# Optimization experiments

Measured on AMD Instinct MI355X. Metric: run time of the kernel, lower is better.

## Reference

```python
import jax, jax.numpy as jnp
import numpy as np

BS, NA, NE, NAL = 512, 8, 8, 7        # batch, agents, enemies, allies
OWN_F, EN_F, AL_F = 16, 16, 16        # per-entity feature dims
H, HEADS, HYPER, OUT_N = 64, 4, 64, 6 # rnn_hidden_dim, hpn heads, hyper hidden, normal actions
D_E = (EN_F * H + H + 1) * HEADS      # hypernet-enemy out: input-layer W + fc2 W + fc2 b (per head)
D_A = AL_F * H * HEADS                # hypernet-ally out: input-layer W only (non-MMM map)


def setup_inputs() -> dict:
    key = jax.random.key(0)
    ks = jax.random.split(key, 16)
    def w(k, shape, fan):
        return jax.random.normal(k, shape, jnp.float32) / np.sqrt(fan)
    n = BS * NA
    return dict(
        own_feats=jax.random.normal(ks[0], (n, OWN_F), jnp.float32),
        enemy_feats=jax.random.normal(ks[1], (n * NE, EN_F), jnp.float32),
        ally_feats=jax.random.normal(ks[2], (n * NAL, AL_F), jnp.float32),
        hidden_state=jax.random.normal(ks[3], (n, H), jnp.float32),
        fc1_w=w(ks[4], (OWN_F, H), OWN_F), fc1_b=jnp.zeros((H,), jnp.float32),
        he_w1=w(ks[5], (EN_F, HYPER), EN_F), he_b1=jnp.zeros((HYPER,), jnp.float32),
        he_w2=w(ks[6], (HYPER, D_E), HYPER), he_b2=jnp.zeros((D_E,), jnp.float32),
        ha_w1=w(ks[7], (AL_F, HYPER), AL_F), ha_b1=jnp.zeros((HYPER,), jnp.float32),
        ha_w2=w(ks[8], (HYPER, D_A), HYPER), ha_b2=jnp.zeros((D_A,), jnp.float32),
        w_in_merge=jnp.full((HEADS, H), 1.0 / HEADS, jnp.float32),
        gru_w_ih=w(ks[9], (3 * H, H), H), gru_b_ih=jnp.zeros((3 * H,), jnp.float32),
        gru_w_hh=w(ks[10], (3 * H, H), H), gru_b_hh=jnp.zeros((3 * H,), jnp.float32),
        fc2_w=w(ks[11], (H, OUT_N), H), fc2_b=jnp.zeros((OUT_N,), jnp.float32),
        w_out_merge=jnp.full((HEADS,), 1.0 / HEADS, jnp.float32),
    )


def reference(own_feats, enemy_feats, ally_feats, hidden_state,
              fc1_w, fc1_b, he_w1, he_b1, he_w2, he_b2,
              ha_w1, ha_b1, ha_w2, ha_b2, w_in_merge,
              gru_w_ih, gru_b_ih, gru_w_hh, gru_b_hh,
              fc2_w, fc2_b, w_out_merge):
    n = own_feats.shape[0]  # bs * n_agents
    # --- hypernetworks (per-entity MLPs generating weights) ---
    hyper_e = jax.nn.relu(enemy_feats @ he_w1 + he_b1) @ he_w2 + he_b2  # (n*NE, D_E)
    hyper_a = jax.nn.relu(ally_feats @ ha_w1 + ha_b1) @ ha_w2 + ha_b2   # (n*NAL, D_A)
    # --- permutation-invariant input embedding: generated input weights, sum over entities ---
    w1_e = hyper_e[:, :EN_F * H * HEADS].reshape(n, NE, EN_F, H, HEADS)
    emb_e = jnp.einsum('nef,nefhk->nhk', enemy_feats.reshape(n, NE, EN_F), w1_e)
    w1_a = hyper_a.reshape(n, NAL, AL_F, H, HEADS)
    emb_a = jnp.einsum('naf,nafhk->nhk', ally_feats.reshape(n, NAL, AL_F), w1_a)
    merged = jnp.einsum('nhk,kh->nh', emb_e + emb_a, w_in_merge)  # Merger over heads
    embedding = own_feats @ fc1_w + fc1_b + merged
    x = jax.nn.relu(embedding)
    # --- GRUCell (torch semantics) ---
    gi = x @ gru_w_ih.T + gru_b_ih
    gh = hidden_state @ gru_w_hh.T + gru_b_hh
    ir, iz, ig = jnp.split(gi, 3, axis=-1)
    hr, hz, hg = jnp.split(gh, 3, axis=-1)
    r = jax.nn.sigmoid(ir + hr)
    z = jax.nn.sigmoid(iz + hz)
    g = jnp.tanh(ig + r * hg)
    hh = (1.0 - z) * g + z * hidden_state  # (n, H)
    # --- normal-action Q head ---
    q_normal = (hh @ fc2_w + fc2_b).reshape(BS, NA, OUT_N)
    # --- attack Q: generated per-enemy fc2 weights/bias, tiny batched GEMV + head merge ---
    w2 = hyper_e[:, -(H + 1) * HEADS:-HEADS].reshape(n, NE, H, HEADS)
    b2 = hyper_e[:, -HEADS:].reshape(n, NE, HEADS)
    q_attacks = jnp.einsum('nh,nehk->nek', hh, w2) + b2  # (n, NE, HEADS)
    q_attack = (q_attacks @ w_out_merge).reshape(BS, NA, NE)  # unify_output_heads
    q = jnp.concatenate([q_normal, q_attack], axis=-1)
    return q.reshape(BS, NA, -1), hh.reshape(BS, NA, H)
```

## Files before the change

kernel.cpp:

```cpp
#include <hip/hip_runtime.h>
#include <math.h>

#define NAGT 4096
#define NE 8
#define NAL 7
#define H 64
#define D_E 4356
#define D_A 4096
#define QTOT (NAGT*14)

#define KPAD 2112
#define SPLITS 11
#define KSPL 192
#define BK 64
#define BM 64

#define WBIG_OFF 0
#define WBIG_SZ (KPAD*64)
#define PCAT_OFF (WBIG_OFF + WBIG_SZ)
#define PCAT_SZ (NAGT*KPAD)
#define RELU_OFF (PCAT_OFF + PCAT_SZ)
#define RELU_SZ (NAGT*NE*64)
#define CPART_OFF (RELU_OFF + RELU_SZ)
#define CPART_SZ (SPLITS*NAGT*64)
#define WIHT_OFF (CPART_OFF + CPART_SZ)
#define WIHT_SZ (64*192)
#define WHHT_OFF (WIHT_OFF + WIHT_SZ)
#define WATT_OFF (WHHT_OFF + WIHT_SZ)
#define WATTB_OFF (WATT_OFF + 4096)
#define BATTT_OFF (WATTB_OFF + 64)
#define BATT0_OFF (BATTT_OFF + 64)

#define PREP_ITEMS (WBIG_SZ + 2*WIHT_SZ + 4096 + 64 + 64 + 1)
#define PREP_BLOCKS ((PREP_ITEMS + 255)/256)
#define ENT_BLOCKS (NAGT/4)

__device__ __forceinline__ float dot4w(const float* __restrict__ p,
                                       const float* __restrict__ wim, int h) {
    return p[0]*wim[h] + p[1]*wim[64+h] + p[2]*wim[128+h] + p[3]*wim[192+h];
}

__global__ __launch_bounds__(256) void k_prep_entity(
    const float* __restrict__ own,  const float* __restrict__ ef,
    const float* __restrict__ af,   const float* __restrict__ hew1,
    const float* __restrict__ heb1, const float* __restrict__ hew2,
    const float* __restrict__ heb2, const float* __restrict__ haw1,
    const float* __restrict__ hab1, const float* __restrict__ haw2,
    const float* __restrict__ hab2, const float* __restrict__ wim,
    const float* __restrict__ wih,  const float* __restrict__ whh,
    const float* __restrict__ wom,  const float* __restrict__ fc1w,
    float* __restrict__ ws)
{
    int bid = blockIdx.x;
    if (bid < PREP_BLOCKS) {
        int idx = bid*256 + threadIdx.x;
        if (idx >= PREP_ITEMS) return;
        if (idx < WBIG_SZ) {
            int rr = idx >> 6, h = idx & 63;
            float s;
            if (rr < 1024) {
                int f = rr >> 6, j = rr & 63;
                s = dot4w(hew2 + (size_t)j*D_E + f*256 + h*4, wim, h);
            } else if (rr < 2048) {
                int r2 = rr - 1024; int f = r2 >> 6, j = r2 & 63;
                s = dot4w(haw2 + (size_t)j*D_A + f*256 + h*4, wim, h);
            } else if (rr < 2064) {
                int f = rr - 2048;
                s = dot4w(heb2 + f*256 + h*4, wim, h);
            } else if (rr < 2080) {
                int f = rr - 2064;
                s = dot4w(hab2 + f*256 + h*4, wim, h);
            } else if (rr < 2096) {
                int f = rr - 2080;
                s = fc1w[f*64 + h];
            } else {
                s = 0.f;
            }
            ws[WBIG_OFF + idx] = s;
            return;
        }
        int k2 = idx - WBIG_SZ;
        if (k2 < WIHT_SZ) {
            int h = k2 / 192, c = k2 % 192;
            ws[WIHT_OFF + k2] = wih[c*64 + h];
            return;
        }
        k2 -= WIHT_SZ;
        if (k2 < WIHT_SZ) {
            int h = k2 / 192, c = k2 % 192;
            ws[WHHT_OFF + k2] = whh[c*64 + h];
            return;
        }
        k2 -= WIHT_SZ;
        if (k2 < 4096) {
            int h = k2 >> 6, j = k2 & 63;
            float s = 0.f;
            #pragma unroll
            for (int k = 0; k < 4; k++)
                s = fmaf(wom[k], hew2[(size_t)j*D_E + 4096 + h*4 + k], s);
            ws[WATT_OFF + k2] = s;
            return;
        }
        k2 -= 4096;
        if (k2 < 64) {
            int j = k2;
            float s = 0.f;
            #pragma unroll
            for (int k = 0; k < 4; k++)
                s = fmaf(wom[k], hew2[(size_t)j*D_E + 4352 + k], s);
            ws[WATTB_OFF + j] = s;
            return;
        }
        k2 -= 64;
        if (k2 < 64) {
            int h = k2;
            float s = 0.f;
            #pragma unroll
            for (int k = 0; k < 4; k++)
                s = fmaf(wom[k], heb2[4096 + h*4 + k], s);
            ws[BATTT_OFF + h] = s;
            return;
        }
        {
            float s = 0.f;
            #pragma unroll
            for (int k = 0; k < 4; k++) s = fmaf(wom[k], heb2[4352 + k], s);
            ws[BATT0_OFF] = s;
        }
        return;
    }

    int t = threadIdx.x, w = t >> 6, l = t & 63;
    int n = (bid - PREP_BLOCKS)*4 + w;
    float* pc = ws + PCAT_OFF + (size_t)n*KPAD;

    {
        float Pe[16];
        #pragma unroll
        for (int f = 0; f < 16; f++) Pe[f] = 0.f;
        float se = 0.f;
        for (int e = 0; e < NE; e++) {
            int m = n*NE + e;
            float val = ef[(size_t)m*16 + (l & 15)];
            float ff[16];
            #pragma unroll
            for (int f = 0; f < 16; f++) ff[f] = __shfl(val, f);
            float acc = heb1[l];
            #pragma unroll
            for (int f = 0; f < 16; f++) acc = fmaf(ff[f], hew1[f*64 + l], acc);
            float r = fmaxf(acc, 0.f);
            ws[RELU_OFF + (size_t)m*64 + l] = r;
            #pragma unroll
            for (int f = 0; f < 16; f++) Pe[f] = fmaf(ff[f], r, Pe[f]);
            se += val;
        }
        #pragma unroll
        for (int f = 0; f < 16; f++) pc[f*64 + l] = Pe[f];
        if (l < 16) pc[2048 + l] = se;
    }
    {
        float Pa[16];
        #pragma unroll
        for (int f = 0; f < 16; f++) Pa[f] = 0.f;
        float sa = 0.f;
        for (int a = 0; a < NAL; a++) {
            int m = n*NAL + a;
            float val = af[(size_t)m*16 + (l & 15)];
            float ff[16];
            #pragma unroll
            for (int f = 0; f < 16; f++) ff[f] = __shfl(val, f);
            float acc = hab1[l];
            #pragma unroll
            for (int f = 0; f < 16; f++) acc = fmaf(ff[f], haw1[f*64 + l], acc);
            float r = fmaxf(acc, 0.f);
            #pragma unroll
            for (int f = 0; f < 16; f++) Pa[f] = fmaf(ff[f], r, Pa[f]);
            sa += val;
        }
        #pragma unroll
        for (int f = 0; f < 16; f++) pc[1024 + f*64 + l] = Pa[f];
        if (l < 16) pc[2064 + l] = sa;
    }
    if (l < 16) pc[2080 + l] = own[(size_t)n*16 + l];
    if (l < 16) pc[2096 + l] = 0.f;
}

__global__ __launch_bounds__(256) void k_gemm(const float* __restrict__ wsr,
                                              float* __restrict__ wsw)
{
    __shared__ float As[BK][68];
    __shared__ float Bs[BK][68];
    int t = threadIdx.x;
    int mt = blockIdx.x / SPLITS;
    int sp = blockIdx.x % SPLITS;
    int n0 = mt * BM;
    const float* A = wsr + PCAT_OFF;
    const float* B = wsr + WBIG_OFF;
    float acc[4][4] = {{0.f}};
    int i = t & 15, jq = t >> 4;

    for (int ch = 0; ch < KSPL/BK; ch++) {
        int kb = sp*KSPL + ch*BK;
        #pragma unroll
        for (int li = 0; li < 4; li++) {
            int idx = t + li*256;
            int r = idx >> 4, c = idx & 15;
            float4 v = *(const float4*)(A + (size_t)(n0 + r)*KPAD + kb + c*4);
            int col = ((((r >> 2) ^ c) & 15) << 2) | (r & 3);
            As[c*4 + 0][col] = v.x; As[c*4 + 1][col] = v.y;
            As[c*4 + 2][col] = v.z; As[c*4 + 3][col] = v.w;
            float4 bv = *(const float4*)(B + (size_t)(kb + r)*64 + c*4);
            *(float4*)&Bs[r][c*4] = bv;
        }
        __syncthreads();
        #pragma unroll 16
        for (int kk = 0; kk < BK; kk++) {
            int ga = ((i ^ (kk >> 2)) & 15) << 2;
            float4 a4 = *(const float4*)&As[kk][ga];
            float4 b4 = *(const float4*)&Bs[kk][jq*4];
            float av[4] = {a4.x, a4.y, a4.z, a4.w};
            float bv[4] = {b4.x, b4.y, b4.z, b4.w};
            #pragma unroll
            for (int r = 0; r < 4; r++)
                #pragma unroll
                for (int c = 0; c < 4; c++)
                    acc[r][c] = fmaf(av[r], bv[c], acc[r][c]);
        }
        __syncthreads();
    }
    float* C = wsw + CPART_OFF + (size_t)sp*(NAGT*64);
    #pragma unroll
    for (int qi = 0; qi < 4; qi++) {
        float4 st = make_float4(acc[qi][0], acc[qi][1], acc[qi][2], acc[qi][3]);
        *(float4*)(C + (size_t)(n0 + i*4 + qi)*64 + jq*4) = st;
    }
}

__global__ __launch_bounds__(256) void k_epilogue(
    const float* __restrict__ hidden, const float* __restrict__ fc1b,
    const float* __restrict__ gbih,   const float* __restrict__ gbhh,
    const float* __restrict__ fc2w,   const float* __restrict__ fc2b,
    const float* __restrict__ ws,     float* __restrict__ out)
{
    __shared__ float lX[4][2][64], lH[4][2][64], lHH[4][2][64], lU[4][2][64];
    int t = threadIdx.x, w = t >> 6, j = t & 63;
    int n0 = (blockIdx.x*4 + w)*2;
    const float* Cp = ws + CPART_OFF;

    float hid[2];
    #pragma unroll
    for (int q = 0; q < 2; q++) {
        int n = n0 + q;
        float emb = fc1b[j];
        #pragma unroll
        for (int sp = 0; sp < SPLITS; sp++)
            emb += Cp[(size_t)sp*(NAGT*64) + (size_t)n*64 + j];
        float xv = fmaxf(emb, 0.f);
        lX[w][q][j] = xv;
        float hv = hidden[(size_t)n*64 + j];
        hid[q] = hv; lH[w][q][j] = hv;
    }

    float gir[2], giz[2], gig[2], ghr[2], ghz[2], ghg[2];
    #pragma unroll
    for (int q = 0; q < 2; q++) {
        gir[q] = gbih[j]; giz[q] = gbih[64 + j]; gig[q] = gbih[128 + j];
        ghr[q] = gbhh[j]; ghz[q] = gbhh[64 + j]; ghg[q] = gbhh[128 + j];
    }
    const float* WihT = ws + WIHT_OFF;
    const float* WhhT = ws + WHHT_OFF;
    #pragma unroll 8
    for (int h = 0; h < 64; h++) {
        float wri = WihT[h*192 + j], wzi = WihT[h*192 + 64 + j], wgi = WihT[h*192 + 128 + j];
        float wrh = WhhT[h*192 + j], wzh = WhhT[h*192 + 64 + j], wgh = WhhT[h*192 + 128 + j];
        #pragma unroll
        for (int q = 0; q < 2; q++) {
            float xv = lX[w][q][h], hv = lH[w][q][h];
            gir[q] = fmaf(xv, wri, gir[q]); giz[q] = fmaf(xv, wzi, giz[q]);
            gig[q] = fmaf(xv, wgi, gig[q]);
            ghr[q] = fmaf(hv, wrh, ghr[q]); ghz[q] = fmaf(hv, wzh, ghz[q]);
            ghg[q] = fmaf(hv, wgh, ghg[q]);
        }
    }
    #pragma unroll
    for (int q = 0; q < 2; q++) {
        float r = 1.f/(1.f + expf(-(gir[q] + ghr[q])));
        float z = 1.f/(1.f + expf(-(giz[q] + ghz[q])));
        float g = tanhf(gig[q] + r*ghg[q]);
        float hv = (1.f - z)*g + z*hid[q];
        lHH[w][q][j] = hv;
        out[QTOT + (size_t)(n0 + q)*64 + j] = hv;
    }

    const float* WattT = ws + WATT_OFF;
    float b0 = ws[BATT0_OFF];
    float u[2], cb[2];
    #pragma unroll
    for (int q = 0; q < 2; q++) { u[q] = ws[WATTB_OFF + j]; cb[q] = b0; }
    #pragma unroll 8
    for (int h = 0; h < 64; h++) {
        float wa = WattT[h*64 + j];
        float bt = ws[BATTT_OFF + h];
        #pragma unroll
        for (int q = 0; q < 2; q++) {
            float hv = lHH[w][q][h];
            u[q]  = fmaf(hv, wa, u[q]);
            cb[q] = fmaf(hv, bt, cb[q]);
        }
    }
    #pragma unroll
    for (int q = 0; q < 2; q++) lU[w][q][j] = u[q];

    int e = j >> 3, p = j & 7;
    #pragma unroll
    for (int q = 0; q < 2; q++) {
        int n = n0 + q, m = n*NE + e;
        const float* rl = ws + RELU_OFF + (size_t)m*64 + p*8;
        float4 r0 = *(const float4*)(rl);
        float4 r1 = *(const float4*)(rl + 4);
        float s = 0.f;
        s = fmaf(r0.x, lU[w][q][p*8 + 0], s); s = fmaf(r0.y, lU[w][q][p*8 + 1], s);
        s = fmaf(r0.z, lU[w][q][p*8 + 2], s); s = fmaf(r0.w, lU[w][q][p*8 + 3], s);
        s = fmaf(r1.x, lU[w][q][p*8 + 4], s); s = fmaf(r1.y, lU[w][q][p*8 + 5], s);
        s = fmaf(r1.z, lU[w][q][p*8 + 6], s); s = fmaf(r1.w, lU[w][q][p*8 + 7], s);
        s += __shfl_xor(s, 1); s += __shfl_xor(s, 2); s += __shfl_xor(s, 4);
        if (p == 0) out[(size_t)n*14 + 6 + e] = s + cb[q];
    }
    if (j < 12) {
        int q = j / 6, o = j % 6;
        float qn = fc2b[o];
        #pragma unroll 8
        for (int h = 0; h < 64; h++) qn = fmaf(lHH[w][q][h], fc2w[h*6 + o], qn);
        out[(size_t)(n0 + q)*14 + o] = qn;
    }
}

extern "C" void kernel_launch(void* const* d_in, const int* in_sizes, int n_in,
                              void* d_out, int out_size, void* d_ws, size_t ws_size,
                              hipStream_t stream) {
    const float* own   = (const float*)d_in[0];
    const float* ef    = (const float*)d_in[1];
    const float* af    = (const float*)d_in[2];
    const float* hidden= (const float*)d_in[3];
    const float* fc1w  = (const float*)d_in[4];
    const float* fc1b  = (const float*)d_in[5];
    const float* hew1  = (const float*)d_in[6];
    const float* heb1  = (const float*)d_in[7];
    const float* hew2  = (const float*)d_in[8];
    const float* heb2  = (const float*)d_in[9];
    const float* haw1  = (const float*)d_in[10];
    const float* hab1  = (const float*)d_in[11];
    const float* haw2  = (const float*)d_in[12];
    const float* hab2  = (const float*)d_in[13];
    const float* wim   = (const float*)d_in[14];
    const float* wih   = (const float*)d_in[15];
    const float* gbih  = (const float*)d_in[16];
    const float* whh   = (const float*)d_in[17];
    const float* gbhh  = (const float*)d_in[18];
    const float* fc2w  = (const float*)d_in[19];
    const float* fc2b  = (const float*)d_in[20];
    const float* wom   = (const float*)d_in[21];
    float* out = (float*)d_out;
    float* ws  = (float*)d_ws;

    k_prep_entity<<<PREP_BLOCKS + ENT_BLOCKS, 256, 0, stream>>>(
        own, ef, af, hew1, heb1, hew2, heb2, haw1, hab1, haw2, hab2,
        wim, wih, whh, wom, fc1w, ws);
    k_gemm<<<(NAGT/BM)*SPLITS, 256, 0, stream>>>(ws, ws);
    k_epilogue<<<NAGT/8, 256, 0, stream>>>(hidden, fc1b, gbih, gbhh,
                                           fc2w, fc2b, ws, out);
}
```

Before: 155.8 us.

## Fuse entity hypernet, split-K GEMM and GRU epilogue into one per-block kernel

Replaces the entity-prep, split-K GEMM and epilogue kernels with a single fused kernel. Each 256-thread block handles 8 agents and keeps relu activations, the P-concat rows and the embedding partials in LDS instead of global workspace, then runs the GRU and Q heads in place. This removes the large PCAT, RELU and CPART workspace round-trips and one kernel launch. In exchange the embedding GEMM becomes a per-block GEMV-like loop that streams the full 2112x64 weight matrix per block through L2, and there is less parallelism (512 blocks) with heavy LDS use.

Measured after the change: 174.4 us. +12.0%, slower.

```diff
diff --git a/kernel.cpp b/kernel.cpp
--- a/kernel.cpp
+++ b/kernel.cpp
@@ -4,26 +4,14 @@
 #define NAGT 4096
 #define NE 8
 #define NAL 7
-#define H 64
+#define QTOT (NAGT*14)
 #define D_E 4356
 #define D_A 4096
-#define QTOT (NAGT*14)
-
 #define KPAD 2112
-#define SPLITS 11
-#define KSPL 192
-#define BK 64
-#define BM 64
 
 #define WBIG_OFF 0
 #define WBIG_SZ (KPAD*64)
-#define PCAT_OFF (WBIG_OFF + WBIG_SZ)
-#define PCAT_SZ (NAGT*KPAD)
-#define RELU_OFF (PCAT_OFF + PCAT_SZ)
-#define RELU_SZ (NAGT*NE*64)
-#define CPART_OFF (RELU_OFF + RELU_SZ)
-#define CPART_SZ (SPLITS*NAGT*64)
-#define WIHT_OFF (CPART_OFF + CPART_SZ)
+#define WIHT_OFF (WBIG_OFF + WBIG_SZ)
 #define WIHT_SZ (64*192)
 #define WHHT_OFF (WIHT_OFF + WIHT_SZ)
 #define WATT_OFF (WHHT_OFF + WIHT_SZ)
@@ -33,305 +21,289 @@
 
 #define PREP_ITEMS (WBIG_SZ + 2*WIHT_SZ + 4096 + 64 + 64 + 1)
 #define PREP_BLOCKS ((PREP_ITEMS + 255)/256)
-#define ENT_BLOCKS (NAGT/4)
 
 __device__ __forceinline__ float dot4w(const float* __restrict__ p,
                                        const float* __restrict__ wim, int h) {
     return p[0]*wim[h] + p[1]*wim[64+h] + p[2]*wim[128+h] + p[3]*wim[192+h];
 }
 
-__global__ __launch_bounds__(256) void k_prep_entity(
+__global__ __launch_bounds__(256) void k_prep(
+    const float* __restrict__ hew2, const float* __restrict__ heb2,
+    const float* __restrict__ haw2, const float* __restrict__ hab2,
+    const float* __restrict__ wim,  const float* __restrict__ wih,
+    const float* __restrict__ whh,  const float* __restrict__ wom,
+    const float* __restrict__ fc1w, float* __restrict__ ws)
+{
+    int idx = blockIdx.x*256 + threadIdx.x;
+    if (idx >= PREP_ITEMS) return;
+    if (idx < WBIG_SZ) {
+        int rr = idx >> 6, h = idx & 63;
+        float s;
+        if (rr < 1024) {
+            int f = rr >> 6, j = rr & 63;
+            s = dot4w(hew2 + (size_t)j*D_E + f*256 + h*4, wim, h);
+        } else if (rr < 2048) {
+            int r2 = rr - 1024; int f = r2 >> 6, j = r2 & 63;
+            s = dot4w(haw2 + (size_t)j*D_A + f*256 + h*4, wim, h);
+        } else if (rr < 2064) {
+            s = dot4w(heb2 + (rr - 2048)*256 + h*4, wim, h);
+        } else if (rr < 2080) {
+            s = dot4w(hab2 + (rr - 2064)*256 + h*4, wim, h);
+        } else if (rr < 2096) {
+            s = fc1w[(rr - 2080)*64 + h];
+        } else {
+            s = 0.f;
+        }
+        ws[WBIG_OFF + idx] = s;
+        return;
+    }
+    int k2 = idx - WBIG_SZ;
+    if (k2 < WIHT_SZ) {
+        int h = k2 / 192, c = k2 % 192;
+        ws[WIHT_OFF + k2] = wih[c*64 + h];
+        return;
+    }
+    k2 -= WIHT_SZ;
+    if (k2 < WIHT_SZ) {
+        int h = k2 / 192, c = k2 % 192;
+        ws[WHHT_OFF + k2] = whh[c*64 + h];
+        return;
+    }
+    k2 -= WIHT_SZ;
+    if (k2 < 4096) {
+        int h = k2 >> 6, j = k2 & 63;
+        float s = 0.f;
+        #pragma unroll
+        for (int k = 0; k < 4; k++)
+            s = fmaf(wom[k], hew2[(size_t)j*D_E + 4096 + h*4 + k], s);
+        ws[WATT_OFF + k2] = s;
+        return;
+    }
+    k2 -= 4096;
+    if (k2 < 64) {
+        int j = k2;
+        float s = 0.f;
+        #pragma unroll
+        for (int k = 0; k < 4; k++)
+            s = fmaf(wom[k], hew2[(size_t)j*D_E + 4352 + k], s);
+        ws[WATTB_OFF + j] = s;
+        return;
+    }
+    k2 -= 64;
+    if (k2 < 64) {
+        int h = k2;
+        float s = 0.f;
+        #pragma unroll
+        for (int k = 0; k < 4; k++)
+            s = fmaf(wom[k], heb2[4096 + h*4 + k], s);
+        ws[BATTT_OFF + h] = s;
+        return;
+    }
+    {
+        float s = 0.f;
+        #pragma unroll
+        for (int k = 0; k < 4; k++) s = fmaf(wom[k], heb2[4352 + k], s);
+        ws[BATT0_OFF] = s;
+    }
+}
+
+struct SM {
+    float relu_e[8][8][64];
+    float relu_a[8][7][64];
+    float ef_l[8][8][16];
+    float af_l[8][7][16];
+    float tails[8][64];
+    float pa_lds[4][8][64];
+    float embp[4][8][64];
+    float lH[8][64];
+    float lHH[8][64];
+    float lU[8][64];
+};
+
+__global__ __launch_bounds__(256) void k_fused(
     const float* __restrict__ own,  const float* __restrict__ ef,
-    const float* __restrict__ af,   const float* __restrict__ hew1,
-    const float* __restrict__ heb1, const float* __restrict__ hew2,
-    const float* __restrict__ heb2, const float* __restrict__ haw1,
-    const float* __restrict__ hab1, const float* __restrict__ haw2,
-    const float* __restrict__ hab2, const float* __restrict__ wim,
-    const float* __restrict__ wih,  const float* __restrict__ whh,
-    const float* __restrict__ wom,  const float* __restrict__ fc1w,
-    float* __restrict__ ws)
+    const float* __restrict__ af,   const float* __restrict__ hidden,
+    const float* __restrict__ fc1b, const float* __restrict__ heb1,
+    const float* __restrict__ hew1, const float* __restrict__ hab1,
+    const float* __restrict__ haw1, const float* __restrict__ gbih,
+    const float* __restrict__ gbhh, const float* __restrict__ fc2w,
+    const float* __restrict__ fc2b, const float* __restrict__ ws,
+    float* __restrict__ out)
 {
-    int bid = blockIdx.x;
-    if (bid < PREP_BLOCKS) {
-        int idx = bid*256 + threadIdx.x;
-        if (idx >= PREP_ITEMS) return;
-        if (idx < WBIG_SZ) {
-            int rr = idx >> 6, h = idx & 63;
-            float s;
-            if (rr < 1024) {
-                int f = rr >> 6, j = rr & 63;
-                s = dot4w(hew2 + (size_t)j*D_E + f*256 + h*4, wim, h);
-            } else if (rr < 2048) {
-                int r2 = rr - 1024; int f = r2 >> 6, j = r2 & 63;
-                s = dot4w(haw2 + (size_t)j*D_A + f*256 + h*4, wim, h);
-            } else if (rr < 2064) {
-                int f = rr - 2048;
-                s = dot4w(heb2 + f*256 + h*4, wim, h);
-            } else if (rr < 2080) {
-                int f = rr - 2064;
-                s = dot4w(hab2 + f*256 + h*4, wim, h);
-            } else if (rr < 2096) {
-                int f = rr - 2080;
-                s = fc1w[f*64 + h];
+    __shared__ SM sm;
+    int bid = blockIdx.x, t = threadIdx.x;
+    int w = t >> 6, l = t & 63;
+    int n0 = bid * 8;
+
+    ((float4*)sm.ef_l)[t] = ((const float4*)(ef + (size_t)n0*128))[t];
+    if (t < 224) ((float4*)sm.af_l)[t] = ((const float4*)(af + (size_t)n0*112))[t];
+    if (t < 128) {
+        int a = t >> 4, f = t & 15;
+        sm.tails[a][32+f] = own[(size_t)n0*16 + t];
+        sm.tails[a][48+f] = 0.f;
+        ((float4*)sm.lH)[t] = ((const float4*)(hidden + (size_t)n0*64))[t];
+    }
+    __syncthreads();
+
+    for (int i = 0; i < 30; i++) {
+        int r = w*30 + i;
+        int a = r / 15, ent = r % 15;
+        if (ent < 8) {
+            float accv = heb1[l];
+            #pragma unroll
+            for (int f = 0; f < 16; f++)
+                accv = fmaf(sm.ef_l[a][ent][f], hew1[f*64 + l], accv);
+            sm.relu_e[a][ent][l] = fmaxf(accv, 0.f);
+        } else {
+            int al = ent - 8;
+            float accv = hab1[l];
+            #pragma unroll
+            for (int f = 0; f < 16; f++)
+                accv = fmaf(sm.af_l[a][al][f], haw1[f*64 + l], accv);
+            sm.relu_a[a][al][l] = fmaxf(accv, 0.f);
+        }
+    }
+    if (t < 128) {
+        int a = t >> 4, f = t & 15;
+        float se = 0.f, sa = 0.f;
+        #pragma unroll
+        for (int e = 0; e < 8; e++) se += sm.ef_l[a][e][f];
+        #pragma unroll
+        for (int e = 0; e < 7; e++) sa += sm.af_l[a][e][f];
+        sm.tails[a][f] = se;
+        sm.tails[a][16+f] = sa;
+    }
+    __syncthreads();
+
+    float acc[8];
+    #pragma unroll
+    for (int a = 0; a < 8; a++) acc[a] = 0.f;
+    const float* Wb = ws + WBIG_OFF;
+    for (int rr = w; rr < 33; rr += 4) {
+        #pragma unroll 2
+        for (int a = 0; a < 8; a++) {
+            float pa;
+            if (rr < 16) {
+                pa = 0.f;
+                #pragma unroll
+                for (int e = 0; e < 8; e++)
+                    pa = fmaf(sm.ef_l[a][e][rr], sm.relu_e[a][e][l], pa);
+            } else if (rr < 32) {
+                pa = 0.f;
+                #pragma unroll
+                for (int e = 0; e < 7; e++)
+                    pa = fmaf(sm.af_l[a][e][rr-16], sm.relu_a[a][e][l], pa);
             } else {
-                s = 0.f;
+                pa = sm.tails[a][l];
             }
-            ws[WBIG_OFF + idx] = s;
-            return;
-        }
-        int k2 = idx - WBIG_SZ;
-        if (k2 < WIHT_SZ) {
-            int h = k2 / 192, c = k2 % 192;
-            ws[WIHT_OFF + k2] = wih[c*64 + h];
-            return;
-        }
-        k2 -= WIHT_SZ;
-        if (k2 < WIHT_SZ) {
-            int h = k2 / 192, c = k2 % 192;
-            ws[WHHT_OFF + k2] = whh[c*64 + h];
-            return;
-        }
-        k2 -= WIHT_SZ;
-        if (k2 < 4096) {
-            int h = k2 >> 6, j = k2 & 63;
+            sm.pa_lds[w][a][l] = pa;
+        }
+        const float* wbase = Wb + rr*4096 + l;
+        #pragma unroll 4
+        for (int k4 = 0; k4 < 16; k4++) {
+            float wb0 = wbase[(k4*4+0)*64];
+            float wb1 = wbase[(k4*4+1)*64];
+            float wb2 = wbase[(k4*4+2)*64];
+            float wb3 = wbase[(k4*4+3)*64];
+            #pragma unroll
+            for (int a = 0; a < 8; a++) {
+                float4 pa4 = *(const float4*)&sm.pa_lds[w][a][k4*4];
+                acc[a] = fmaf(pa4.x, wb0, acc[a]);
+                acc[a] = fmaf(pa4.y, wb1, acc[a]);
+                acc[a] = fmaf(pa4.z, wb2, acc[a]);
+                acc[a] = fmaf(pa4.w, wb3, acc[a]);
+            }
+        }
+    }
+    #pragma unroll
+    for (int a = 0; a < 8; a++) sm.embp[w][a][l] = acc[a];
+    __syncthreads();
+
+    #pragma unroll
+    for (int ii = 0; ii < 2; ii++) {
+        int idx = t + ii*256;
+        int a = idx >> 6, h = idx & 63;
+        float emb = fc1b[h];
+        #pragma unroll
+        for (int sw = 0; sw < 4; sw++) emb += sm.embp[sw][a][h];
+        sm.embp[0][a][h] = fmaxf(emb, 0.f);
+    }
+    __syncthreads();
+
+    {
+        int a0 = w*2;
+        float hid[2], gir[2], giz[2], gig[2], ghr[2], ghz[2], ghg[2];
+        #pragma unroll
+        for (int q = 0; q < 2; q++) {
+            hid[q] = sm.lH[a0+q][l];
+            gir[q] = gbih[l]; giz[q] = gbih[64+l]; gig[q] = gbih[128+l];
+            ghr[q] = gbhh[l]; ghz[q] = gbhh[64+l]; ghg[q] = gbhh[128+l];
+        }
+        const float* WihT = ws + WIHT_OFF;
+        const float* WhhT = ws + WHHT_OFF;
+        #pragma unroll 8
+        for (int h = 0; h < 64; h++) {
+            float wri = WihT[h*192 + l], wzi = WihT[h*192 + 64 + l], wgi = WihT[h*192 + 128 + l];
+            float wrh = WhhT[h*192 + l], wzh = WhhT[h*192 + 64 + l], wgh = WhhT[h*192 + 128 + l];
+            #pragma unroll
+            for (int q = 0; q < 2; q++) {
+                float xv = sm.embp[0][a0+q][h], hv = sm.lH[a0+q][h];
+                gir[q] = fmaf(xv, wri, gir[q]); giz[q] = fmaf(xv, wzi, giz[q]);
+                gig[q] = fmaf(xv, wgi, gig[q]);
+                ghr[q] = fmaf(hv, wrh, ghr[q]); ghz[q] = fmaf(hv, wzh, ghz[q]);
+                ghg[q] = fmaf(hv, wgh, ghg[q]);
+            }
+        }
+        #pragma unroll
+        for (int q = 0; q < 2; q++) {
+            float r = 1.f/(1.f + expf(-(gir[q] + ghr[q])));
+            float z = 1.f/(1.f + expf(-(giz[q] + ghz[q])));
+            float g = tanhf(gig[q] + r*ghg[q]);
+            float hv = (1.f - z)*g + z*hid[q];
+            sm.lHH[a0+q][l] = hv;
+            out[QTOT + (size_t)(n0 + a0 + q)*64 + l] = hv;
+        }
+
+        const float* WattT = ws + WATT_OFF;
+        float b0 = ws[BATT0_OFF];
+        float u[2], cb[2];
+        #pragma unroll
+        for (int q = 0; q < 2; q++) { u[q] = ws[WATTB_OFF + l]; cb[q] = b0; }
+        #pragma unroll 8
+        for (int h = 0; h < 64; h++) {
+            float wa = WattT[h*64 + l];
+            float bt = ws[BATTT_OFF + h];
+            #pragma unroll
+            for (int q = 0; q < 2; q++) {
+                float hv = sm.lHH[a0+q][h];
+                u[q]  = fmaf(hv, wa, u[q]);
+                cb[q] = fmaf(hv, bt, cb[q]);
+            }
+        }
+        #pragma unroll
+        for (int q = 0; q < 2; q++) sm.lU[a0+q][l] = u[q];
+
+        int e = l >> 3, p = l & 7;
+        #pragma unroll
+        for (int q = 0; q < 2; q++) {
+            int a = a0 + q, n = n0 + a;
+            float4 r0 = *(const float4*)&sm.relu_e[a][e][p*8];
+            float4 r1 = *(const float4*)&sm.relu_e[a][e][p*8 + 4];
             float s = 0.f;
-            #pragma unroll
-            for (int k = 0; k < 4; k++)
-                s = fmaf(wom[k], hew2[(size_t)j*D_E + 4096 + h*4 + k], s);
-            ws[WATT_OFF + k2] = s;
-            return;
-        }
-        k2 -= 4096;
-        if (k2 < 64) {
-            int j = k2;
-            float s = 0.f;
-            #pragma unroll
-            for (int k = 0; k < 4; k++)
-                s = fmaf(wom[k], hew2[(size_t)j*D_E + 4352 + k], s);
-            ws[WATTB_OFF + j] = s;
-            return;
-        }
-        k2 -= 64;
-        if (k2 < 64) {
-            int h = k2;
-            float s = 0.f;
-            #pragma unroll
-            for (int k = 0; k < 4; k++)
-                s = fmaf(wom[k], heb2[4096 + h*4 + k], s);
-            ws[BATTT_OFF + h] = s;
-            return;
-        }
-        {
-            float s = 0.f;
-            #pragma unroll
-            for (int k = 0; k < 4; k++) s = fmaf(wom[k], heb2[4352 + k], s);
-            ws[BATT0_OFF] = s;
-        }
-        return;
-    }
-
-    int t = threadIdx.x, w = t >> 6, l = t & 63;
-    int n = (bid - PREP_BLOCKS)*4 + w;
-    float* pc = ws + PCAT_OFF + (size_t)n*KPAD;
-
-    {
-        float Pe[16];
-        #pragma unroll
-        for (int f = 0; f < 16; f++) Pe[f] = 0.f;
-        float se = 0.f;
-        for (int e = 0; e < NE; e++) {
-            int m = n*NE + e;
-            float val = ef[(size_t)m*16 + (l & 15)];
-            float ff[16];
-            #pragma unroll
-            for (int f = 0; f < 16; f++) ff[f] = __shfl(val, f);
-            float acc = heb1[l];
-            #pragma unroll
-            for (int f = 0; f < 16; f++) acc = fmaf(ff[f], hew1[f*64 + l], acc);
-            float r = fmaxf(acc, 0.f);
-            ws[RELU_OFF + (size_t)m*64 + l] = r;
-            #pragma unroll
-            for (int f = 0; f < 16; f++) Pe[f] = fmaf(ff[f], r, Pe[f]);
-            se += val;
-        }
-        #pragma unroll
-        for (int f = 0; f < 16; f++) pc[f*64 + l] = Pe[f];
-        if (l < 16) pc[2048 + l] = se;
-    }
-    {
-        float Pa[16];
-        #pragma unroll
-        for (int f = 0; f < 16; f++) Pa[f] = 0.f;
-        float sa = 0.f;
-        for (int a = 0; a < NAL; a++) {
-            int m = n*NAL + a;
-            float val = af[(size_t)m*16 + (l & 15)];
-            float ff[16];
-            #pragma unroll
-            for (int f = 0; f < 16; f++) ff[f] = __shfl(val, f);
-            float acc = hab1[l];
-            #pragma unroll
-            for (int f = 0; f < 16; f++) acc = fmaf(ff[f], haw1[f*64 + l], acc);
-            float r = fmaxf(acc, 0.f);
-            #pragma unroll
-            for (int f = 0; f < 16; f++) Pa[f] = fmaf(ff[f], r, Pa[f]);
-            sa += val;
-        }
-        #pragma unroll
-        for (int f = 0; f < 16; f++) pc[1024 + f*64 + l] = Pa[f];
-        if (l < 16) pc[2064 + l] = sa;
-    }
-    if (l < 16) pc[2080 + l] = own[(size_t)n*16 + l];
-    if (l < 16) pc[2096 + l] = 0.f;
-}
-
-__global__ __launch_bounds__(256) void k_gemm(const float* __restrict__ wsr,
-                                              float* __restrict__ wsw)
-{
-    __shared__ float As[BK][68];
-    __shared__ float Bs[BK][68];
-    int t = threadIdx.x;
-    int mt = blockIdx.x / SPLITS;
-    int sp = blockIdx.x % SPLITS;
-    int n0 = mt * BM;
-    const float* A = wsr + PCAT_OFF;
-    const float* B = wsr + WBIG_OFF;
-    float acc[4][4] = {{0.f}};
-    int i = t & 15, jq = t >> 4;
-
-    for (int ch = 0; ch < KSPL/BK; ch++) {
-        int kb = sp*KSPL + ch*BK;
-        #pragma unroll
-        for (int li = 0; li < 4; li++) {
-            int idx = t + li*256;
-            int r = idx >> 4, c = idx & 15;
-            float4 v = *(const float4*)(A + (size_t)(n0 + r)*KPAD + kb + c*4);
-            int col = ((((r >> 2) ^ c) & 15) << 2) | (r & 3);
-            As[c*4 + 0][col] = v.x; As[c*4 + 1][col] = v.y;
-            As[c*4 + 2][col] = v.z; As[c*4 + 3][col] = v.w;
-            float4 bv = *(const float4*)(B + (size_t)(kb + r)*64 + c*4);
-            *(float4*)&Bs[r][c*4] = bv;
-        }
-        __syncthreads();
-        #pragma unroll 16
-        for (int kk = 0; kk < BK; kk++) {
-            int ga = ((i ^ (kk >> 2)) & 15) << 2;
-            float4 a4 = *(const float4*)&As[kk][ga];
-            float4 b4 = *(const float4*)&Bs[kk][jq*4];
-            float av[4] = {a4.x, a4.y, a4.z, a4.w};
-            float bv[4] = {b4.x, b4.y, b4.z, b4.w};
-            #pragma unroll
-            for (int r = 0; r < 4; r++)
-                #pragma unroll
-                for (int c = 0; c < 4; c++)
-                    acc[r][c] = fmaf(av[r], bv[c], acc[r][c]);
-        }
-        __syncthreads();
-    }
-    float* C = wsw + CPART_OFF + (size_t)sp*(NAGT*64);
-    #pragma unroll
-    for (int qi = 0; qi < 4; qi++) {
-        float4 st = make_float4(acc[qi][0], acc[qi][1], acc[qi][2], acc[qi][3]);
-        *(float4*)(C + (size_t)(n0 + i*4 + qi)*64 + jq*4) = st;
-    }
-}
-
-__global__ __launch_bounds__(256) void k_epilogue(
-    const float* __restrict__ hidden, const float* __restrict__ fc1b,
-    const float* __restrict__ gbih,   const float* __restrict__ gbhh,
-    const float* __restrict__ fc2w,   const float* __restrict__ fc2b,
-    const float* __restrict__ ws,     float* __restrict__ out)
-{
-    __shared__ float lX[4][2][64], lH[4][2][64], lHH[4][2][64], lU[4][2][64];
-    int t = threadIdx.x, w = t >> 6, j = t & 63;
-    int n0 = (blockIdx.x*4 + w)*2;
-    const float* Cp = ws + CPART_OFF;
-
-    float hid[2];
-    #pragma unroll
-    for (int q = 0; q < 2; q++) {
-        int n = n0 + q;
-        float emb = fc1b[j];
-        #pragma unroll
-        for (int sp = 0; sp < SPLITS; sp++)
-            emb += Cp[(size_t)sp*(NAGT*64) + (size_t)n*64 + j];
-        float xv = fmaxf(emb, 0.f);
-        lX[w][q][j] = xv;
-        float hv = hidden[(size_t)n*64 + j];
-        hid[q] = hv; lH[w][q][j] = hv;
-    }
-
-    float gir[2], giz[2], gig[2], ghr[2], ghz[2], ghg[2];
-    #pragma unroll
-    for (int q = 0; q < 2; q++) {
-        gir[q] = gbih[j]; giz[q] = gbih[64 + j]; gig[q] = gbih[128 + j];
-        ghr[q] = gbhh[j]; ghz[q] = gbhh[64 + j]; ghg[q] = gbhh[128 + j];
-    }
-    const float* WihT = ws + WIHT_OFF;
-    const float* WhhT = ws + WHHT_OFF;
-    #pragma unroll 8
-    for (int h = 0; h < 64; h++) {
-        float wri = WihT[h*192 + j], wzi = WihT[h*192 + 64 + j], wgi = WihT[h*192 + 128 + j];
-        float wrh = WhhT[h*192 + j], wzh = WhhT[h*192 + 64 + j], wgh = WhhT[h*192 + 128 + j];
-        #pragma unroll
-        for (int q = 0; q < 2; q++) {
-            float xv = lX[w][q][h], hv = lH[w][q][h];
-            gir[q] = fmaf(xv, wri, gir[q]); giz[q] = fmaf(xv, wzi, giz[q]);
-            gig[q] = fmaf(xv, wgi, gig[q]);
-            ghr[q] = fmaf(hv, wrh, ghr[q]); ghz[q] = fmaf(hv, wzh, ghz[q]);
-            ghg[q] = fmaf(hv, wgh, ghg[q]);
-        }
-    }
-    #pragma unroll
-    for (int q = 0; q < 2; q++) {
-        float r = 1.f/(1.f + expf(-(gir[q] + ghr[q])));
-        float z = 1.f/(1.f + expf(-(giz[q] + ghz[q])));
-        float g = tanhf(gig[q] + r*ghg[q]);
-        float hv = (1.f - z)*g + z*hid[q];
-        lHH[w][q][j] = hv;
-        out[QTOT + (size_t)(n0 + q)*64 + j] = hv;
-    }
-
-    const float* WattT = ws + WATT_OFF;
-    float b0 = ws[BATT0_OFF];
-    float u[2], cb[2];
-    #pragma unroll
-    for (int q = 0; q < 2; q++) { u[q] = ws[WATTB_OFF + j]; cb[q] = b0; }
-    #pragma unroll 8
-    for (int h = 0; h < 64; h++) {
-        float wa = WattT[h*64 + j];
-        float bt = ws[BATTT_OFF + h];
-        #pragma unroll
-        for (int q = 0; q < 2; q++) {
-            float hv = lHH[w][q][h];
-            u[q]  = fmaf(hv, wa, u[q]);
-            cb[q] = fmaf(hv, bt, cb[q]);
-        }
-    }
-    #pragma unroll
-    for (int q = 0; q < 2; q++) lU[w][q][j] = u[q];
-
-    int e = j >> 3, p = j & 7;
-    #pragma unroll
-    for (int q = 0; q < 2; q++) {
-        int n = n0 + q, m = n*NE + e;
-        const float* rl = ws + RELU_OFF + (size_t)m*64 + p*8;
-        float4 r0 = *(const float4*)(rl);
-        float4 r1 = *(const float4*)(rl + 4);
-        float s = 0.f;
-        s = fmaf(r0.x, lU[w][q][p*8 + 0], s); s = fmaf(r0.y, lU[w][q][p*8 + 1], s);
-        s = fmaf(r0.z, lU[w][q][p*8 + 2], s); s = fmaf(r0.w, lU[w][q][p*8 + 3], s);
-        s = fmaf(r1.x, lU[w][q][p*8 + 4], s); s = fmaf(r1.y, lU[w][q][p*8 + 5], s);
-        s = fmaf(r1.z, lU[w][q][p*8 + 6], s); s = fmaf(r1.w, lU[w][q][p*8 + 7], s);
-        s += __shfl_xor(s, 1); s += __shfl_xor(s, 2); s += __shfl_xor(s, 4);
-        if (p == 0) out[(size_t)n*14 + 6 + e] = s + cb[q];
-    }
-    if (j < 12) {
-        int q = j / 6, o = j % 6;
-        float qn = fc2b[o];
-        #pragma unroll 8
-        for (int h = 0; h < 64; h++) qn = fmaf(lHH[w][q][h], fc2w[h*6 + o], qn);
-        out[(size_t)(n0 + q)*14 + o] = qn;
+            s = fmaf(r0.x, sm.lU[a][p*8 + 0], s); s = fmaf(r0.y, sm.lU[a][p*8 + 1], s);
+            s = fmaf(r0.z, sm.lU[a][p*8 + 2], s); s = fmaf(r0.w, sm.lU[a][p*8 + 3], s);
+            s = fmaf(r1.x, sm.lU[a][p*8 + 4], s); s = fmaf(r1.y, sm.lU[a][p*8 + 5], s);
+            s = fmaf(r1.z, sm.lU[a][p*8 + 6], s); s = fmaf(r1.w, sm.lU[a][p*8 + 7], s);
+            s += __shfl_xor(s, 1); s += __shfl_xor(s, 2); s += __shfl_xor(s, 4);
+            if (p == 0) out[(size_t)n*14 + 6 + e] = s + cb[q];
+        }
+        if (l < 12) {
+            int q = l / 6, o = l % 6;
+            float qn = fc2b[o];
+            #pragma unroll 8
+            for (int h = 0; h < 64; h++) qn = fmaf(sm.lHH[a0+q][h], fc2w[h*6 + o], qn);
+            out[(size_t)(n0 + a0 + q)*14 + o] = qn;
+        }
     }
 }
 
@@ -363,10 +335,9 @@
     float* out = (float*)d_out;
     float* ws  = (float*)d_ws;
 
-    k_prep_entity<<<PREP_BLOCKS + ENT_BLOCKS, 256, 0, stream>>>(
-        own, ef, af, hew1, heb1, hew2, heb2, haw1, hab1, haw2, hab2,
-        wim, wih, whh, wom, fc1w, ws);
-    k_gemm<<<(NAGT/BM)*SPLITS, 256, 0, stream>>>(ws, ws);
-    k_epilogue<<<NAGT/8, 256, 0, stream>>>(hidden, fc1b, gbih, gbhh,
-                                           fc2w, fc2b, ws, out);
+    k_prep<<<PREP_BLOCKS, 256, 0, stream>>>(hew2, heb2, haw2, hab2, wim,
+                                            wih, whh, wom, fc1w, ws);
+    k_fused<<<NAGT/8, 256, 0, stream>>>(own, ef, af, hidden, fc1b, heb1,
+                                        hew1, hab1, haw1, gbih, gbhh,
+                                        fc2w, fc2b, ws, out);
 }
```
